# Optimization experiments

Hardware: AMD Instinct MI355X
Metric: run time of the kernel (lower is better)

Reference implementation:

```python
import jax, jax.numpy as jnp
import numpy as np

N = 262144      # total nodes
G = 256         # graphs
P = 1024        # nodes per graph (k=None sort pool keeps all)
E = 4194304     # edges
F_IN = 128
H = 32
C = 10          # out capsules / classes
OUT_LEN = 16
IN_LEN = 96     # 3 * 32 concat
NUM_ITERS = 3


def setup_inputs() -> dict:
    key = jax.random.key(0)
    ks = jax.random.split(key, 12)
    x = jax.random.normal(ks[0], (N, F_IN), jnp.float32)
    # edges within each graph of size P
    src = jax.random.randint(ks[1], (E,), 0, N)
    off = jax.random.randint(ks[2], (E,), 0, P)
    dst = (src // P) * P + off
    edge_index = jnp.stack([src, dst]).astype(jnp.int64)
    batch = jnp.repeat(jnp.arange(G), P).astype(jnp.int64)
    W1 = jax.random.normal(ks[3], (F_IN, H), jnp.float32) / np.sqrt(F_IN)
    b1 = jnp.zeros((H,), jnp.float32)
    W2 = jax.random.normal(ks[4], (H, H), jnp.float32) / np.sqrt(H)
    b2 = jnp.zeros((H,), jnp.float32)
    W3 = jax.random.normal(ks[5], (H, H), jnp.float32) / np.sqrt(H)
    b3 = jnp.zeros((H,), jnp.float32)
    caps_W = jax.random.normal(ks[6], (C, OUT_LEN, IN_LEN), jnp.float32) * 0.05
    return {"x": x, "edge_index": edge_index, "batch": batch,
            "W1": W1, "b1": b1, "W2": W2, "b2": b2, "W3": W3, "b3": b3,
            "caps_W": caps_W}


def _position_encoding(length, dim):
    pos = jnp.arange(length, dtype=jnp.float32)[:, None]
    i = jnp.arange(dim // 2, dtype=jnp.float32)[None, :]
    ang = pos / jnp.power(10000.0, 2.0 * i / dim)
    return jnp.stack([jnp.sin(ang), jnp.cos(ang)], axis=-1).reshape(length, dim)


def _squash(v, eps=1e-12):
    n2 = jnp.sum(v * v, axis=-1, keepdims=True)
    return (n2 / (1.0 + n2)) * v / jnp.sqrt(n2 + eps)


def reference(x, edge_index, batch, W1, b1, W2, b2, W3, b3, caps_W):
    src, dst = edge_index[0], edge_index[1]
    # remove_self_loops, then GCNConv re-adds self loops with weight 1
    mask = (src != dst).astype(x.dtype)
    deg = jax.ops.segment_sum(mask, dst, num_segments=N) + 1.0
    dis = jax.lax.rsqrt(deg)                         # deg^{-1/2}
    enorm = dis[src] * dis[dst] * mask               # [E]

    def gcn(h, W, b):
        h = h @ W                                    # [N,H]
        agg = jax.ops.segment_sum(h[src] * enorm[:, None], dst, num_segments=N)
        agg = agg + h * (dis * dis)[:, None]         # self-loop term deg^{-1}
        return jnp.tanh(agg + b)

    x1 = gcn(x, W1, b1)
    x2 = gcn(x1, W2, b2)
    x3 = gcn(x2, W3, b3)
    h = jnp.concatenate([x1, x2, x3], axis=-1)       # [N, 96]

    # global_sort_pool (k=None): per-graph sort by last channel, descending
    hg = h.reshape(G, P, IN_LEN)
    order = jnp.argsort(-hg[:, :, -1], axis=1)
    hs = jnp.take_along_axis(hg, order[:, :, None], axis=1)  # [G,P,96]
    hs = hs + _position_encoding(P, IN_LEN)[None]

    # CapsuleLinear, shared weight: priors [G, C, P, OUT_LEN]
    priors = jnp.einsum('oji,gki->gokj', caps_W, hs)

    # k-means routing
    v = jnp.mean(priors, axis=2, keepdims=True)      # [G,C,1,OUT_LEN]
    for _ in range(NUM_ITERS):
        vn = v / (jnp.linalg.norm(v, axis=-1, keepdims=True) + 1e-12)
        logits = jnp.sum(priors * vn, axis=-1, keepdims=True)  # [G,C,P,1]
        prob = jax.nn.softmax(logits, axis=2)
        v = jnp.sum(prob * priors, axis=2, keepdims=True)
    out = _squash(v)[:, :, 0, :]                     # [G, C, OUT_LEN]
    return jnp.linalg.norm(out, axis=-1)             # [G, C]
```

## Files before the change

### kernel.cpp

```cpp
#include <hip/hip_runtime.h>
#include <hip/hip_fp16.h>
#include <cstdint>
#include <cstddef>

#define N_NODES   262144
#define NG        256
#define PP        1024
#define NE        4194304
#define FIN       128
#define HH        32
#define NC        10
#define OL        16
#define IL        96
#define NITER     3
#define ECHUNK    4096
#define NCHUNK    (NE/ECHUNK)
#define ECAP      18432

typedef _Float16 half8 __attribute__((ext_vector_type(8)));
typedef float f32x4 __attribute__((ext_vector_type(4)));

__device__ __forceinline__ float tanh_fast(float x) {
  float e = __expf(2.0f * x);
  return 1.0f - 2.0f / (e + 1.0f);
}
__device__ __forceinline__ unsigned pk2(float a, float b) {
  __half2 h = __floats2half2_rn(a, b);
  union { __half2 h; unsigned u; } v; v.h = h; return v.u;
}
__device__ __forceinline__ __half2 u2h2(unsigned u) {
  union { unsigned u; __half2 h; } v; v.u = u; return v.h;
}

__device__ __forceinline__ int hslc(int row, int c) {
  return row * 32 + ((c ^ ((row >> 1) & 3)) << 3);
}
__device__ __forceinline__ int hslh(int row, int halfcol) {
  return hslc(row, halfcol >> 3) + (halfcol & 7);
}

__global__ void k_hist(const int* __restrict__ ei, unsigned* __restrict__ histT) {
  __shared__ unsigned lh[NG];
  int t = threadIdx.x, b = blockIdx.x;
  lh[t] = 0;
  __syncthreads();
  int base = b * ECHUNK;
  for (int q = t; q < ECHUNK; q += 256) {
    int e = base + q;
    int s = ei[e], d = ei[NE + e];
    if (s != d) atomicAdd(&lh[s >> 10], 1u);
  }
  __syncthreads();
  histT[t * NCHUNK + b] = lh[t];
}

__global__ void k_scanA(const unsigned* __restrict__ histT, unsigned* __restrict__ cbaseT,
                        unsigned* __restrict__ gtot) {
  __shared__ unsigned wtot[4];
  int t = threadIdx.x, g = blockIdx.x;
  int lane = t & 63, wv = t >> 6;
  uint4 hv = *(const uint4*)(histT + (size_t)g * NCHUNK + t * 4);
  unsigned s0 = hv.x, s1 = s0 + hv.y, s2 = s1 + hv.z, s3 = s2 + hv.w;
  unsigned tsum = s3, sc = tsum;
  for (int d = 1; d < 64; d <<= 1) {
    unsigned v = __shfl_up(sc, d, 64);
    if (lane >= d) sc += v;
  }
  if (lane == 63) wtot[wv] = sc;
  __syncthreads();
  unsigned woff = 0;
  for (int w = 0; w < wv; ++w) woff += wtot[w];
  unsigned base = woff + sc - tsum;
  cbaseT[(size_t)(t * 4 + 0) * NG + g] = base;
  cbaseT[(size_t)(t * 4 + 1) * NG + g] = base + s0;
  cbaseT[(size_t)(t * 4 + 2) * NG + g] = base + s1;
  cbaseT[(size_t)(t * 4 + 3) * NG + g] = base + s2;
  if (t == 255) gtot[g] = woff + sc;
}

__global__ void k_scanB(const unsigned* __restrict__ gtot, unsigned* __restrict__ gbase) {
  __shared__ unsigned wtot[4];
  int t = threadIdx.x;
  int lane = t & 63, wv = t >> 6;
  unsigned x = gtot[t], sc = x;
  for (int d = 1; d < 64; d <<= 1) {
    unsigned v = __shfl_up(sc, d, 64);
    if (lane >= d) sc += v;
  }
  if (lane == 63) wtot[wv] = sc;
  __syncthreads();
  unsigned woff = 0;
  for (int w = 0; w < wv; ++w) woff += wtot[w];
  gbase[t] = woff + sc - x;
  if (t == 255) gbase[256] = woff + sc;
}

__global__ void k_scatter(const int* __restrict__ ei, const unsigned* __restrict__ cbaseT,
                          const unsigned* __restrict__ gbase, unsigned* __restrict__ epack) {
  __shared__ unsigned lcur[NG];
  int t = threadIdx.x, b = blockIdx.x;
  lcur[t] = gbase[t] + cbaseT[(size_t)b * NG + t];
  __syncthreads();
  int base = b * ECHUNK;
  for (int q = t; q < ECHUNK; q += 256) {
    int e = base + q;
    int s = ei[e], d = ei[NE + e];
    if (s != d) {
      int g = s >> 10;
      unsigned pos = atomicAdd(&lcur[g], 1u);
      epack[pos] = (unsigned)(s & 1023) | ((unsigned)(d & 1023) << 10);
    }
  }
}

__global__ __launch_bounds__(256) void k_dstsort(const unsigned* __restrict__ epack,
                          const unsigned* __restrict__ gbase,
                          unsigned short* __restrict__ esrc16,
                          unsigned* __restrict__ dstptr) {
  __shared__ unsigned shist[PP];
  __shared__ unsigned wsum[256];
  __shared__ unsigned cur[PP];
  int t = threadIdx.x, g = blockIdx.x;
  unsigned e0 = gbase[g], e1 = gbase[g + 1];
  for (int i = t; i < PP; i += 256) shist[i] = 0;
  __syncthreads();
  for (unsigned e = e0 + t; e < e1; e += 256)
    atomicAdd(&shist[(epack[e] >> 10) & 1023], 1u);
  __syncthreads();
  unsigned h0 = shist[4 * t], h1 = shist[4 * t + 1], h2 = shist[4 * t + 2], h3 = shist[4 * t + 3];
  unsigned tsum = h0 + h1 + h2 + h3;
  wsum[t] = tsum;
  __syncthreads();
  for (int off = 1; off < 256; off <<= 1) {
    unsigned v = (t >= off) ? wsum[t - off] : 0u;
    __syncthreads();
    wsum[t] += v;
    __syncthreads();
  }
  unsigned excl = wsum[t] - tsum;
  unsigned c0 = excl, c1 = c0 + h0, c2 = c1 + h1, c3 = c2 + h2;
  cur[4 * t] = c0; cur[4 * t + 1] = c1; cur[4 * t + 2] = c2; cur[4 * t + 3] = c3;
  unsigned* dp = dstptr + (size_t)g * (PP + 1);
  dp[4 * t] = c0; dp[4 * t + 1] = c1; dp[4 * t + 2] = c2; dp[4 * t + 3] = c3;
  if (t == 0) dp[PP] = e1 - e0;
  __syncthreads();
  unsigned short* eg = esrc16 + (size_t)g * ECAP;
  for (unsigned e = e0 + t; e < e1; e += 256) {
    unsigned pk = epack[e];
    unsigned so = pk & 1023, dofs = (pk >> 10) & 1023;
    unsigned pos = atomicAdd(&cur[dofs], 1u);
    if (pos < ECAP) eg[pos] = (unsigned short)so;
  }
}

__global__ void k_dis(const unsigned* __restrict__ dstptr, float* __restrict__ dis) {
  int n = blockIdx.x * 256 + threadIdx.x;
  int g = n >> 10, k = n & 1023;
  const unsigned* dp = dstptr + (size_t)g * (PP + 1) + k;
  float deg = (float)(dp[1] - dp[0]);
  dis[n] = 1.0f / sqrtf(deg + 1.0f);
}

__device__ __forceinline__ void gcn_layer(__half* hsl, const float* dg, const unsigned* dp,
                                          const unsigned short* eg, const float* bias,
                                          int coloff, const float* Wn, __half* hb16,
                                          float* keyArr, int t) {
  unsigned xnu[2][16];
#pragma unroll
  for (int pth = 0; pth < 2; ++pth) {
    int k = t + pth * 512;
    float dk = dg[k];
    unsigned e0 = dp[k], e1 = dp[k + 1];
    if (e1 > (unsigned)ECAP) e1 = ECAP;
    __half2 acc2[16];
    {
      uint4 u0 = *(const uint4*)&hsl[hslc(k, 0)];
      uint4 u1 = *(const uint4*)&hsl[hslc(k, 1)];
      uint4 u2 = *(const uint4*)&hsl[hslc(k, 2)];
      uint4 u3 = *(const uint4*)&hsl[hslc(k, 3)];
      acc2[0] = u2h2(u0.x); acc2[1] = u2h2(u0.y); acc2[2] = u2h2(u0.z); acc2[3] = u2h2(u0.w);
      acc2[4] = u2h2(u1.x); acc2[5] = u2h2(u1.y); acc2[6] = u2h2(u1.z); acc2[7] = u2h2(u1.w);
      acc2[8] = u2h2(u2.x); acc2[9] = u2h2(u2.y); acc2[10] = u2h2(u2.z); acc2[11] = u2h2(u2.w);
      acc2[12] = u2h2(u3.x); acc2[13] = u2h2(u3.y); acc2[14] = u2h2(u3.z); acc2[15] = u2h2(u3.w);
    }
    unsigned e = e0;
    for (; e + 1 < e1; e += 2) {
      int s0 = eg[e], s1 = eg[e + 1];
      uint4 a0 = *(const uint4*)&hsl[hslc(s0, 0)];
      uint4 a1 = *(const uint4*)&hsl[hslc(s0, 1)];
      uint4 a2 = *(const uint4*)&hsl[hslc(s0, 2)];
      uint4 a3 = *(const uint4*)&hsl[hslc(s0, 3)];
      uint4 b0 = *(const uint4*)&hsl[hslc(s1, 0)];
      uint4 b1 = *(const uint4*)&hsl[hslc(s1, 1)];
      uint4 b2 = *(const uint4*)&hsl[hslc(s1, 2)];
      uint4 b3 = *(const uint4*)&hsl[hslc(s1, 3)];
      acc2[0] = __hadd2(acc2[0], __hadd2(u2h2(a0.x), u2h2(b0.x)));
      acc2[1] = __hadd2(acc2[1], __hadd2(u2h2(a0.y), u2h2(b0.y)));
      acc2[2] = __hadd2(acc2[2], __hadd2(u2h2(a0.z), u2h2(b0.z)));
      acc2[3] = __hadd2(acc2[3], __hadd2(u2h2(a0.w), u2h2(b0.w)));
      acc2[4] = __hadd2(acc2[4], __hadd2(u2h2(a1.x), u2h2(b1.x)));
      acc2[5] = __hadd2(acc2[5], __hadd2(u2h2(a1.y), u2h2(b1.y)));
      acc2[6] = __hadd2(acc2[6], __hadd2(u2h2(a1.z), u2h2(b1.z)));
      acc2[7] = __hadd2(acc2[7], __hadd2(u2h2(a1.w), u2h2(b1.w)));
      acc2[8] = __hadd2(acc2[8], __hadd2(u2h2(a2.x), u2h2(b2.x)));
      acc2[9] = __hadd2(acc2[9], __hadd2(u2h2(a2.y), u2h2(b2.y)));
      acc2[10] = __hadd2(acc2[10], __hadd2(u2h2(a2.z), u2h2(b2.z)));
      acc2[11] = __hadd2(acc2[11], __hadd2(u2h2(a2.w), u2h2(b2.w)));
      acc2[12] = __hadd2(acc2[12], __hadd2(u2h2(a3.x), u2h2(b3.x)));
      acc2[13] = __hadd2(acc2[13], __hadd2(u2h2(a3.y), u2h2(b3.y)));
      acc2[14] = __hadd2(acc2[14], __hadd2(u2h2(a3.z), u2h2(b3.z)));
      acc2[15] = __hadd2(acc2[15], __hadd2(u2h2(a3.w), u2h2(b3.w)));
    }
    if (e < e1) {
      int s0 = eg[e];
      uint4 a0 = *(const uint4*)&hsl[hslc(s0, 0)];
      uint4 a1 = *(const uint4*)&hsl[hslc(s0, 1)];
      uint4 a2 = *(const uint4*)&hsl[hslc(s0, 2)];
      uint4 a3 = *(const uint4*)&hsl[hslc(s0, 3)];
      acc2[0] = __hadd2(acc2[0], u2h2(a0.x)); acc2[1] = __hadd2(acc2[1], u2h2(a0.y));
      acc2[2] = __hadd2(acc2[2], u2h2(a0.z)); acc2[3] = __hadd2(acc2[3], u2h2(a0.w));
      acc2[4] = __hadd2(acc2[4], u2h2(a1.x)); acc2[5] = __hadd2(acc2[5], u2h2(a1.y));
      acc2[6] = __hadd2(acc2[6], u2h2(a1.z)); acc2[7] = __hadd2(acc2[7], u2h2(a1.w));
      acc2[8] = __hadd2(acc2[8], u2h2(a2.x)); acc2[9] = __hadd2(acc2[9], u2h2(a2.y));
      acc2[10] = __hadd2(acc2[10], u2h2(a2.z)); acc2[11] = __hadd2(acc2[11], u2h2(a2.w));
      acc2[12] = __hadd2(acc2[12], u2h2(a3.x)); acc2[13] = __hadd2(acc2[13], u2h2(a3.y));
      acc2[14] = __hadd2(acc2[14], u2h2(a3.z)); acc2[15] = __hadd2(acc2[15], u2h2(a3.w));
    }
    float lastv = 0.f;
#pragma unroll
    for (int i = 0; i < 16; ++i) {
      float2 f = __half22float2(acc2[i]);
      float a0 = tanh_fast(dk * f.x + bias[2 * i]);
      float a1 = tanh_fast(dk * f.y + bias[2 * i + 1]);
      xnu[pth][i] = pk2(a0, a1);
      if (i == 15) lastv = a1;
    }
    __half* hr = hb16 + (size_t)k * IL + coloff;
    uint4 h0, h1;
    h0.x = xnu[pth][0]; h0.y = xnu[pth][1]; h0.z = xnu[pth][2]; h0.w = xnu[pth][3];
    h1.x = xnu[pth][4]; h1.y = xnu[pth][5]; h1.z = xnu[pth][6]; h1.w = xnu[pth][7];
    ((uint4*)hr)[0] = h0;
    ((uint4*)hr)[1] = h1;
    uint4 h2, h3;
    h2.x = xnu[pth][8]; h2.y = xnu[pth][9]; h2.z = xnu[pth][10]; h2.w = xnu[pth][11];
    h3.x = xnu[pth][12]; h3.y = xnu[pth][13]; h3.z = xnu[pth][14]; h3.w = xnu[pth][15];
    ((uint4*)hr)[2] = h2;
    ((uint4*)hr)[3] = h3;
    if (keyArr) keyArr[k] = lastv;
  }
  __syncthreads();
  if (Wn) {
#pragma unroll
    for (int pth = 0; pth < 2; ++pth) {
      int k = t + pth * 512;
      float dk = dg[k];
      float4 o4[8];
#pragma unroll
      for (int j = 0; j < 8; ++j) { o4[j].x = 0.f; o4[j].y = 0.f; o4[j].z = 0.f; o4[j].w = 0.f; }
#pragma unroll
      for (int c2 = 0; c2 < 16; ++c2) {
        float2 xc = __half22float2(u2h2(xnu[pth][c2]));
        const float4* wr0 = (const float4*)(Wn + (2 * c2) * 32);
        const float4* wr1 = (const float4*)(Wn + (2 * c2 + 1) * 32);
#pragma unroll
        for (int j4 = 0; j4 < 8; ++j4) {
          float4 w0 = wr0[j4], w1 = wr1[j4];
          o4[j4].x += xc.x * w0.x + xc.y * w1.x;
          o4[j4].y += xc.x * w0.y + xc.y * w1.y;
          o4[j4].z += xc.x * w0.z + xc.y * w1.z;
          o4[j4].w += xc.x * w0.w + xc.y * w1.w;
        }
      }
#pragma unroll
      for (int c = 0; c < 4; ++c) {
        uint4 u;
        u.x = pk2(o4[2 * c].x * dk, o4[2 * c].y * dk);
        u.y = pk2(o4[2 * c].z * dk, o4[2 * c].w * dk);
        u.z = pk2(o4[2 * c + 1].x * dk, o4[2 * c + 1].y * dk);
        u.w = pk2(o4[2 * c + 1].z * dk, o4[2 * c + 1].w * dk);
        *(uint4*)&hsl[hslc(k, c)] = u;
      }
    }
    __syncthreads();
  }
}

__global__ __launch_bounds__(512, 4) void k_gcn(const float* __restrict__ x,
                                             const float* __restrict__ dis,
                                             const unsigned short* __restrict__ esrc16,
                                             const unsigned* __restrict__ dstptr,
                                             const float* __restrict__ W1, const float* __restrict__ b1,
                                             const float* __restrict__ W2, const float* __restrict__ b2,
                                             const float* __restrict__ W3, const float* __restrict__ b3,
                                             __half* __restrict__ h16, float* __restrict__ key) {
  __shared__ __half hsl[PP * 32];
  int t = threadIdx.x, g = blockIdx.x;
  const float* dg = dis + (size_t)g * PP;
  const unsigned* dp = dstptr + (size_t)g * (PP + 1);
  const unsigned short* eg = esrc16 + (size_t)g * ECAP;
  __half* hb16 = h16 + (size_t)g * PP * IL;
  float* keyg = key + (size_t)g * PP;

  {
    int wv = t >> 6, lane = t & 63, quad = lane >> 4, l16 = lane & 15;
    half8 bfr[2][4];
#pragma unroll
    for (int nt = 0; nt < 2; ++nt)
#pragma unroll
      for (int kf = 0; kf < 4; ++kf) {
        half8 bb;
#pragma unroll
        for (int j = 0; j < 8; ++j)
          bb[j] = (_Float16)W1[(kf * 32 + quad * 8 + j) * HH + nt * 16 + l16];
        bfr[nt][kf] = bb;
      }
#pragma unroll
    for (int rt = 0; rt < 8; ++rt) {
      int row = wv * 128 + rt * 16 + l16;
      const float* xr = x + ((size_t)g * PP + row) * FIN;
      half8 af[4];
#pragma unroll
      for (int kf = 0; kf < 4; ++kf) {
        float4 xa = *(const float4*)(xr + kf * 32 + quad * 8);
        float4 xb = *(const float4*)(xr + kf * 32 + quad * 8 + 4);
        half8 a;
        a[0] = (_Float16)xa.x; a[1] = (_Float16)xa.y; a[2] = (_Float16)xa.z; a[3] = (_Float16)xa.w;
        a[4] = (_Float16)xb.x; a[5] = (_Float16)xb.y; a[6] = (_Float16)xb.z; a[7] = (_Float16)xb.w;
        af[kf] = a;
      }
      int rb = wv * 128 + rt * 16 + quad * 4;
      float dv0 = dg[rb], dv1 = dg[rb + 1], dv2 = dg[rb + 2], dv3 = dg[rb + 3];
#pragma unroll
      for (int nt = 0; nt < 2; ++nt) {
        f32x4 acc = {0.f, 0.f, 0.f, 0.f};
        acc = __builtin_amdgcn_mfma_f32_16x16x32_f16(af[0], bfr[nt][0], acc, 0, 0, 0);
        acc = __builtin_amdgcn_mfma_f32_16x16x32_f16(af[1], bfr[nt][1], acc, 0, 0, 0);
        acc = __builtin_amdgcn_mfma_f32_16x16x32_f16(af[2], bfr[nt][2], acc, 0, 0, 0);
        acc = __builtin_amdgcn_mfma_f32_16x16x32_f16(af[3], bfr[nt][3], acc, 0, 0, 0);
        int col = nt * 16 + l16;
        hsl[hslh(rb + 0, col)] = __float2half(acc[0] * dv0);
        hsl[hslh(rb + 1, col)] = __float2half(acc[1] * dv1);
        hsl[hslh(rb + 2, col)] = __float2half(acc[2] * dv2);
        hsl[hslh(rb + 3, col)] = __float2half(acc[3] * dv3);
      }
    }
  }
  __syncthreads();

  gcn_layer(hsl, dg, dp, eg, b1, 0,  W2, hb16, nullptr, t);
  gcn_layer(hsl, dg, dp, eg, b2, 32, W3, hb16, nullptr, t);
  gcn_layer(hsl, dg, dp, eg, b3, 64, nullptr, hb16, keyg, t);
}

__global__ __launch_bounds__(512) void k_sort(const float* __restrict__ keyArr,
                                              unsigned short* __restrict__ rank16) {
  __shared__ float key[PP];
  __shared__ unsigned sidx[PP];
  int t = threadIdx.x, g = blockIdx.x;
  for (int i = t; i < PP; i += 512) {
    key[i] = keyArr[(size_t)g * PP + i];
    sidx[i] = i;
  }
  __syncthreads();
  for (int sz = 2; sz <= PP; sz <<= 1) {
    for (int st = sz >> 1; st > 0; st >>= 1) {
      int i = 2 * t - (t & (st - 1));
      int j = i + st;
      float ki = key[i], kj = key[j];
      unsigned ii = sidx[i], ij = sidx[j];
      bool less_ji = (kj > ki) || (kj == ki && ij < ii);
      bool asc = ((i & sz) == 0);
      if (less_ji == asc) { key[i] = kj; key[j] = ki; sidx[i] = ij; sidx[j] = ii; }
      __syncthreads();
    }
  }
  for (int i = t; i < PP; i += 512) rank16[g * PP + sidx[i]] = (unsigned short)i;
}

__global__ void k_pe(float* __restrict__ pe) {
  int id = blockIdx.x * 256 + threadIdx.x;
  if (id >= PP * 48) return;
  int pos = id / 48, i = id % 48;
  float denom = powf(10000.0f, (2.0f * i) / 96.0f);
  float ang = (float)pos / denom;
  pe[pos * IL + 2 * i] = sinf(ang);
  pe[pos * IL + 2 * i + 1] = cosf(ang);
}

__global__ void k_wpe(const float* __restrict__ pe, const float* __restrict__ capsW,
                      __half* __restrict__ wpe) {
  int id = blockIdx.x * 256 + threadIdx.x;
  if (id >= NC * PP * OL) return;
  int j = id & 15;
  int pos = (id >> 4) & 1023;
  int c = id >> 14;
  const float* wr = capsW + (size_t)(c * OL + j) * IL;
  const float* pr = pe + (size_t)pos * IL;
  float a = 0;
#pragma unroll 8
  for (int i = 0; i < IL; ++i) a += wr[i] * pr[i];
  wpe[(((size_t)c << 10) + pos) * 16 + j] = __float2half(a);
}

__global__ __launch_bounds__(256) void k_pgemm(const __half* __restrict__ h16,
                                               const float* __restrict__ capsW,
                                               __half* __restrict__ Pc) {
  int t = threadIdx.x, b = blockIdx.x;
  int g = b >> 2;
  int wv = t >> 6, lane = t & 63;
  int quad = lane >> 4, l16 = lane & 15;
  half8 afr[4][3];
#pragma unroll
  for (int rt = 0; rt < 4; ++rt) {
    int row = b * 256 + wv * 64 + rt * 16 + l16;
    const __half* hr = h16 + (size_t)row * IL + quad * 8;
#pragma unroll
    for (int kb = 0; kb < 3; ++kb) {
      uint4 u = *(const uint4*)(hr + kb * 32);
      afr[rt][kb] = __builtin_bit_cast(half8, u);
    }
  }
  int krow_base = (b & 3) * 256 + wv * 64;
  for (int ct = 0; ct < NC; ++ct) {
    half8 bfr[3];
    const float* wr = capsW + (size_t)(ct * 16 + l16) * IL + quad * 8;
#pragma unroll
    for (int kb = 0; kb < 3; ++kb) {
      float4 xx = *(const float4*)(wr + kb * 32);
      float4 yy = *(const float4*)(wr + kb * 32 + 4);
      half8 bb;
      bb[0] = (_Float16)xx.x; bb[1] = (_Float16)xx.y; bb[2] = (_Float16)xx.z; bb[3] = (_Float16)xx.w;
      bb[4] = (_Float16)yy.x; bb[5] = (_Float16)yy.y; bb[6] = (_Float16)yy.z; bb[7] = (_Float16)yy.w;
      bfr[kb] = bb;
    }
#pragma unroll
    for (int rt = 0; rt < 4; ++rt) {
      f32x4 acc = {0.f, 0.f, 0.f, 0.f};
      acc = __builtin_amdgcn_mfma_f32_16x16x32_f16(afr[rt][0], bfr[0], acc, 0, 0, 0);
      acc = __builtin_amdgcn_mfma_f32_16x16x32_f16(afr[rt][1], bfr[1], acc, 0, 0, 0);
      acc = __builtin_amdgcn_mfma_f32_16x16x32_f16(afr[rt][2], bfr[2], acc, 0, 0, 0);
      int krow = krow_base + rt * 16;
      __half* po = Pc + ((((size_t)g * NC + ct) << 10) + krow) * 16 + l16;
#pragma unroll
      for (int r = 0; r < 4; ++r)
        po[(quad * 4 + r) * 16] = __float2half(acc[r]);
    }
  }
}

__global__ __launch_bounds__(256) void k_route2(const __half* __restrict__ Pc,
                                                const __half* __restrict__ wpe,
                                                const unsigned short* __restrict__ rank16,
                                                float* __restrict__ out) {
  __shared__ float v_l[16];
  __shared__ float wred[4][17];
  int t = threadIdx.x;
  int gc = blockIdx.x;
  int g = gc / NC, c = gc - g * NC;
  int lane = t & 63, wv = t >> 6;
  const __half* pg = Pc + ((size_t)gc << 10) * 16;
  const unsigned short* rk = rank16 + (size_t)g * PP;
  const __half* wc = wpe + ((size_t)c << 10) * 16;
  float pr[4][16];
  float vsum[16];
#pragma unroll
  for (int i = 0; i < 16; ++i) vsum[i] = 0.f;
#pragma unroll
  for (int r = 0; r < 4; ++r) {
    int k = t + r * 256;
    uint4 a0 = *(const uint4*)(pg + (size_t)k * 16);
    uint4 a1 = *(const uint4*)(pg + (size_t)k * 16 + 8);
    int rkk = rk[k];
    uint4 b0 = *(const uint4*)(wc + (size_t)rkk * 16);
    uint4 b1 = *(const uint4*)(wc + (size_t)rkk * 16 + 8);
    const __half2* pa0 = (const __half2*)&a0; const __half2* pa1 = (const __half2*)&a1;
    const __half2* pb0 = (const __half2*)&b0; const __half2* pb1 = (const __half2*)&b1;
#pragma unroll
    for (int j = 0; j < 4; ++j) {
      float2 fa = __half22float2(pa0[j]); float2 fb = __half22float2(pb0[j]);
      pr[r][2 * j] = fa.x + fb.x; pr[r][2 * j + 1] = fa.y + fb.y;
      float2 fa1 = __half22float2(pa1[j]); float2 fb1 = __half22float2(pb1[j]);
      pr[r][8 + 2 * j] = fa1.x + fb1.x; pr[r][8 + 2 * j + 1] = fa1.y + fb1.y;
    }
#pragma unroll
    for (int i = 0; i < 16; ++i) vsum[i] += pr[r][i];
  }
#pragma unroll
  for (int d = 1; d < 64; d <<= 1)
#pragma unroll
    for (int i = 0; i < 16; ++i) vsum[i] += __shfl_xor(vsum[i], d, 64);
  if (lane == 0) {
#pragma unroll
    for (int i = 0; i < 16; ++i) wred[wv][i] = vsum[i];
  }
  __syncthreads();
  if (t < 16) v_l[t] = wred[0][t] + wred[1][t] + wred[2][t] + wred[3][t];
  __syncthreads();
  for (int it = 0; it < NITER; ++it) {
    float vn[16]; float n2 = 0;
#pragma unroll
    for (int i = 0; i < 16; ++i) { float x = v_l[i]; vn[i] = x; n2 += x * x; }
    float inv = 1.0f / (sqrtf(n2) + 1e-12f);
#pragma unroll
    for (int i = 0; i < 16; ++i) vn[i] *= inv;
    float lg[4];
#pragma unroll
    for (int r = 0; r < 4; ++r) {
      float a = 0;
#pragma unroll
      for (int i = 0; i < 16; ++i) a += pr[r][i] * vn[i];
      lg[r] = a;
    }
    float mx = fmaxf(fmaxf(lg[0], lg[1]), fmaxf(lg[2], lg[3]));
#pragma unroll
    for (int d = 1; d < 64; d <<= 1) mx = fmaxf(mx, __shfl_xor(mx, d, 64));
    __syncthreads();
    if (lane == 0) wred[wv][16] = mx;
    __syncthreads();
    float gmax = fmaxf(fmaxf(wred[0][16], wred[1][16]), fmaxf(wred[2][16], wred[3][16]));
    float es = 0; float eacc[16];
#pragma unroll
    for (int i = 0; i < 16; ++i) eacc[i] = 0.f;
#pragma unroll
    for (int r = 0; r < 4; ++r) {
      float e = __expf(lg[r] - gmax);
      es += e;
#pragma unroll
      for (int i = 0; i < 16; ++i) eacc[i] += e * pr[r][i];
    }
#pragma unroll
    for (int d = 1; d < 64; d <<= 1) {
      es += __shfl_xor(es, d, 64);
#pragma unroll
      for (int i = 0; i < 16; ++i) eacc[i] += __shfl_xor(eacc[i], d, 64);
    }
    __syncthreads();
    if (lane == 0) {
#pragma unroll
      for (int i = 0; i < 16; ++i) wred[wv][i] = eacc[i];
      wred[wv][16] = es;
    }
    __syncthreads();
    if (t < 16) {
      float s = wred[0][t] + wred[1][t] + wred[2][t] + wred[3][t];
      float S = wred[0][16] + wred[1][16] + wred[2][16] + wred[3][16];
      v_l[t] = s / S;
    }
    __syncthreads();
  }
  if (t == 0) {
    float n2 = 0;
#pragma unroll
    for (int i = 0; i < 16; ++i) { float x = v_l[i]; n2 += x * x; }
    out[gc] = (n2 / (1.0f + n2)) * sqrtf(n2) / sqrtf(n2 + 1e-12f);
  }
}

extern "C" void kernel_launch(void* const* d_in, const int* in_sizes, int n_in,
                              void* d_out, int out_size, void* d_ws, size_t ws_size,
                              hipStream_t stream) {
  const float* x     = (const float*)d_in[0];
  const int*   ei    = (const int*)d_in[1];
  const float* W1    = (const float*)d_in[3];
  const float* b1    = (const float*)d_in[4];
  const float* W2    = (const float*)d_in[5];
  const float* b2    = (const float*)d_in[6];
  const float* W3    = (const float*)d_in[7];
  const float* b3    = (const float*)d_in[8];
  const float* capsW = (const float*)d_in[9];
  float* out = (float*)d_out;

  char* wp = (char*)d_ws;
  auto alloc = [&](size_t bytes) { char* p = wp; wp += (bytes + 255) & ~(size_t)255; return p; };
  float*    dis    = (float*)alloc((size_t)N_NODES * 4);
  __half*   h16    = (__half*)alloc((size_t)N_NODES * IL * 2);
  float*    key    = (float*)alloc((size_t)N_NODES * 4);
  char*     ureg   = wp;
  unsigned* epack  = (unsigned*)alloc((size_t)NE * 4);
  unsigned short* esrc16 = (unsigned short*)alloc((size_t)NG * ECAP * 2);
  unsigned* histT  = (unsigned*)alloc((size_t)NCHUNK * NG * 4);
  unsigned* cbaseT = (unsigned*)alloc((size_t)NCHUNK * NG * 4);
  const size_t PC_BYTES = (size_t)NG * NC * PP * 16 * 2;
  if ((size_t)(wp - ureg) < PC_BYTES) wp = ureg + ((PC_BYTES + 255) & ~(size_t)255);
  __half*   Pc     = (__half*)ureg;
  unsigned* gtot   = (unsigned*)alloc((size_t)NG * 4);
  unsigned* gbase  = (unsigned*)alloc((size_t)(NG + 1) * 4);
  unsigned* dstptr = (unsigned*)alloc((size_t)NG * (PP + 1) * 4);
  unsigned short* rank16 = (unsigned short*)alloc((size_t)NG * PP * 2);
  float*    pe     = (float*)alloc((size_t)PP * IL * 4);
  __half*   wpe    = (__half*)alloc((size_t)NC * PP * OL * 2);

  k_hist<<<NCHUNK, 256, 0, stream>>>(ei, histT);
  k_scanA<<<NG, 256, 0, stream>>>(histT, cbaseT, gtot);
  k_scanB<<<1, 256, 0, stream>>>(gtot, gbase);
  k_scatter<<<NCHUNK, 256, 0, stream>>>(ei, cbaseT, gbase, epack);
  k_dstsort<<<NG, 256, 0, stream>>>(epack, gbase, esrc16, dstptr);
  k_dis<<<N_NODES / 256, 256, 0, stream>>>(dstptr, dis);
  k_pe<<<(PP * 48) / 256, 256, 0, stream>>>(pe);
  k_wpe<<<(NC * PP * OL) / 256, 256, 0, stream>>>(pe, capsW, wpe);

  k_gcn<<<NG, 512, 0, stream>>>(x, dis, esrc16, dstptr, W1, b1, W2, b2, W3, b3, h16, key);

  k_sort<<<NG, 512, 0, stream>>>(key, rank16);
  k_pgemm<<<N_NODES / 256, 256, 0, stream>>>(h16, capsW, Pc);
  k_route2<<<NG * NC, 256, 0, stream>>>(Pc, wpe, rank16, out);
}
```

Before: 654.2 us.

## Split fused per-graph GCN kernel into GEMM plus per-layer aggregation kernels

Replaces the single k_gcn kernel (one 512-thread block per graph running all three layers) with a standalone MFMA GEMM kernel for layer 1 and three aggregation launches. Each aggregation launch uses two blocks per graph, so 512 blocks instead of 256, which fills more compute units. The cost is an extra global round trip: each block reloads the graph's 1024x32 fp16 features into LDS, both half-blocks load the full graph, and the next layer's linear output goes through global memory in ping-pong buffers, one of which aliases the epack scratch. It also adds three extra kernel launches.

```diff
diff --git a/kernel.cpp b/kernel.cpp
--- a/kernel.cpp
+++ b/kernel.cpp
@@ -35,9 +35,6 @@
 __device__ __forceinline__ int hslc(int row, int c) {
   return row * 32 + ((c ^ ((row >> 1) & 3)) << 3);
 }
-__device__ __forceinline__ int hslh(int row, int halfcol) {
-  return hslc(row, halfcol >> 3) + (halfcol & 7);
-}
 
 __global__ void k_hist(const int* __restrict__ ei, unsigned* __restrict__ histT) {
   __shared__ unsigned lh[NG];
@@ -161,195 +158,189 @@
   dis[n] = 1.0f / sqrtf(deg + 1.0f);
 }
 
-__device__ __forceinline__ void gcn_layer(__half* hsl, const float* dg, const unsigned* dp,
-                                          const unsigned short* eg, const float* bias,
-                                          int coloff, const float* Wn, __half* hb16,
-                                          float* keyArr, int t) {
-  unsigned xnu[2][16];
-#pragma unroll
-  for (int pth = 0; pth < 2; ++pth) {
-    int k = t + pth * 512;
-    float dk = dg[k];
-    unsigned e0 = dp[k], e1 = dp[k + 1];
-    if (e1 > (unsigned)ECAP) e1 = ECAP;
-    __half2 acc2[16];
-    {
-      uint4 u0 = *(const uint4*)&hsl[hslc(k, 0)];
-      uint4 u1 = *(const uint4*)&hsl[hslc(k, 1)];
-      uint4 u2 = *(const uint4*)&hsl[hslc(k, 2)];
-      uint4 u3 = *(const uint4*)&hsl[hslc(k, 3)];
-      acc2[0] = u2h2(u0.x); acc2[1] = u2h2(u0.y); acc2[2] = u2h2(u0.z); acc2[3] = u2h2(u0.w);
-      acc2[4] = u2h2(u1.x); acc2[5] = u2h2(u1.y); acc2[6] = u2h2(u1.z); acc2[7] = u2h2(u1.w);
-      acc2[8] = u2h2(u2.x); acc2[9] = u2h2(u2.y); acc2[10] = u2h2(u2.z); acc2[11] = u2h2(u2.w);
-      acc2[12] = u2h2(u3.x); acc2[13] = u2h2(u3.y); acc2[14] = u2h2(u3.z); acc2[15] = u2h2(u3.w);
-    }
-    unsigned e = e0;
-    for (; e + 1 < e1; e += 2) {
-      int s0 = eg[e], s1 = eg[e + 1];
-      uint4 a0 = *(const uint4*)&hsl[hslc(s0, 0)];
-      uint4 a1 = *(const uint4*)&hsl[hslc(s0, 1)];
-      uint4 a2 = *(const uint4*)&hsl[hslc(s0, 2)];
-      uint4 a3 = *(const uint4*)&hsl[hslc(s0, 3)];
-      uint4 b0 = *(const uint4*)&hsl[hslc(s1, 0)];
-      uint4 b1 = *(const uint4*)&hsl[hslc(s1, 1)];
-      uint4 b2 = *(const uint4*)&hsl[hslc(s1, 2)];
-      uint4 b3 = *(const uint4*)&hsl[hslc(s1, 3)];
-      acc2[0] = __hadd2(acc2[0], __hadd2(u2h2(a0.x), u2h2(b0.x)));
-      acc2[1] = __hadd2(acc2[1], __hadd2(u2h2(a0.y), u2h2(b0.y)));
-      acc2[2] = __hadd2(acc2[2], __hadd2(u2h2(a0.z), u2h2(b0.z)));
-      acc2[3] = __hadd2(acc2[3], __hadd2(u2h2(a0.w), u2h2(b0.w)));
-      acc2[4] = __hadd2(acc2[4], __hadd2(u2h2(a1.x), u2h2(b1.x)));
-      acc2[5] = __hadd2(acc2[5], __hadd2(u2h2(a1.y), u2h2(b1.y)));
-      acc2[6] = __hadd2(acc2[6], __hadd2(u2h2(a1.z), u2h2(b1.z)));
-      acc2[7] = __hadd2(acc2[7], __hadd2(u2h2(a1.w), u2h2(b1.w)));
-      acc2[8] = __hadd2(acc2[8], __hadd2(u2h2(a2.x), u2h2(b2.x)));
-      acc2[9] = __hadd2(acc2[9], __hadd2(u2h2(a2.y), u2h2(b2.y)));
-      acc2[10] = __hadd2(acc2[10], __hadd2(u2h2(a2.z), u2h2(b2.z)));
-      acc2[11] = __hadd2(acc2[11], __hadd2(u2h2(a2.w), u2h2(b2.w)));
-      acc2[12] = __hadd2(acc2[12], __hadd2(u2h2(a3.x), u2h2(b3.x)));
-      acc2[13] = __hadd2(acc2[13], __hadd2(u2h2(a3.y), u2h2(b3.y)));
-      acc2[14] = __hadd2(acc2[14], __hadd2(u2h2(a3.z), u2h2(b3.z)));
-      acc2[15] = __hadd2(acc2[15], __hadd2(u2h2(a3.w), u2h2(b3.w)));
-    }
-    if (e < e1) {
-      int s0 = eg[e];
-      uint4 a0 = *(const uint4*)&hsl[hslc(s0, 0)];
-      uint4 a1 = *(const uint4*)&hsl[hslc(s0, 1)];
-      uint4 a2 = *(const uint4*)&hsl[hslc(s0, 2)];
-      uint4 a3 = *(const uint4*)&hsl[hslc(s0, 3)];
-      acc2[0] = __hadd2(acc2[0], u2h2(a0.x)); acc2[1] = __hadd2(acc2[1], u2h2(a0.y));
-      acc2[2] = __hadd2(acc2[2], u2h2(a0.z)); acc2[3] = __hadd2(acc2[3], u2h2(a0.w));
-      acc2[4] = __hadd2(acc2[4], u2h2(a1.x)); acc2[5] = __hadd2(acc2[5], u2h2(a1.y));
-      acc2[6] = __hadd2(acc2[6], u2h2(a1.z)); acc2[7] = __hadd2(acc2[7], u2h2(a1.w));
-      acc2[8] = __hadd2(acc2[8], u2h2(a2.x)); acc2[9] = __hadd2(acc2[9], u2h2(a2.y));
-      acc2[10] = __hadd2(acc2[10], u2h2(a2.z)); acc2[11] = __hadd2(acc2[11], u2h2(a2.w));
-      acc2[12] = __hadd2(acc2[12], u2h2(a3.x)); acc2[13] = __hadd2(acc2[13], u2h2(a3.y));
-      acc2[14] = __hadd2(acc2[14], u2h2(a3.z)); acc2[15] = __hadd2(acc2[15], u2h2(a3.w));
-    }
-    float lastv = 0.f;
-#pragma unroll
-    for (int i = 0; i < 16; ++i) {
-      float2 f = __half22float2(acc2[i]);
-      float a0 = tanh_fast(dk * f.x + bias[2 * i]);
-      float a1 = tanh_fast(dk * f.y + bias[2 * i + 1]);
-      xnu[pth][i] = pk2(a0, a1);
-      if (i == 15) lastv = a1;
-    }
-    __half* hr = hb16 + (size_t)k * IL + coloff;
-    uint4 h0, h1;
-    h0.x = xnu[pth][0]; h0.y = xnu[pth][1]; h0.z = xnu[pth][2]; h0.w = xnu[pth][3];
-    h1.x = xnu[pth][4]; h1.y = xnu[pth][5]; h1.z = xnu[pth][6]; h1.w = xnu[pth][7];
-    ((uint4*)hr)[0] = h0;
-    ((uint4*)hr)[1] = h1;
-    uint4 h2, h3;
-    h2.x = xnu[pth][8]; h2.y = xnu[pth][9]; h2.z = xnu[pth][10]; h2.w = xnu[pth][11];
-    h3.x = xnu[pth][12]; h3.y = xnu[pth][13]; h3.z = xnu[pth][14]; h3.w = xnu[pth][15];
-    ((uint4*)hr)[2] = h2;
-    ((uint4*)hr)[3] = h3;
-    if (keyArr) keyArr[k] = lastv;
-  }
-  __syncthreads();
-  if (Wn) {
-#pragma unroll
-    for (int pth = 0; pth < 2; ++pth) {
-      int k = t + pth * 512;
-      float dk = dg[k];
-      float4 o4[8];
-#pragma unroll
-      for (int j = 0; j < 8; ++j) { o4[j].x = 0.f; o4[j].y = 0.f; o4[j].z = 0.f; o4[j].w = 0.f; }
-#pragma unroll
-      for (int c2 = 0; c2 < 16; ++c2) {
-        float2 xc = __half22float2(u2h2(xnu[pth][c2]));
-        const float4* wr0 = (const float4*)(Wn + (2 * c2) * 32);
-        const float4* wr1 = (const float4*)(Wn + (2 * c2 + 1) * 32);
-#pragma unroll
-        for (int j4 = 0; j4 < 8; ++j4) {
-          float4 w0 = wr0[j4], w1 = wr1[j4];
-          o4[j4].x += xc.x * w0.x + xc.y * w1.x;
-          o4[j4].y += xc.x * w0.y + xc.y * w1.y;
-          o4[j4].z += xc.x * w0.z + xc.y * w1.z;
-          o4[j4].w += xc.x * w0.w + xc.y * w1.w;
-        }
-      }
-#pragma unroll
-      for (int c = 0; c < 4; ++c) {
-        uint4 u;
-        u.x = pk2(o4[2 * c].x * dk, o4[2 * c].y * dk);
-        u.y = pk2(o4[2 * c].z * dk, o4[2 * c].w * dk);
-        u.z = pk2(o4[2 * c + 1].x * dk, o4[2 * c + 1].y * dk);
-        u.w = pk2(o4[2 * c + 1].z * dk, o4[2 * c + 1].w * dk);
-        *(uint4*)&hsl[hslc(k, c)] = u;
-      }
-    }
-    __syncthreads();
-  }
-}
-
-__global__ __launch_bounds__(512, 4) void k_gcn(const float* __restrict__ x,
-                                             const float* __restrict__ dis,
-                                             const unsigned short* __restrict__ esrc16,
-                                             const unsigned* __restrict__ dstptr,
-                                             const float* __restrict__ W1, const float* __restrict__ b1,
-                                             const float* __restrict__ W2, const float* __restrict__ b2,
-                                             const float* __restrict__ W3, const float* __restrict__ b3,
-                                             __half* __restrict__ h16, float* __restrict__ key) {
+__global__ __launch_bounds__(256) void k_gemm1(const float* __restrict__ x,
+                                               const float* __restrict__ dis,
+                                               const float* __restrict__ W1,
+                                               __half* __restrict__ hlin) {
+  int t = threadIdx.x, b = blockIdx.x;
+  int wv = t >> 6, lane = t & 63, quad = lane >> 4, l16 = lane & 15;
+  half8 bfr[2][4];
+#pragma unroll
+  for (int nt = 0; nt < 2; ++nt)
+#pragma unroll
+    for (int kf = 0; kf < 4; ++kf) {
+      half8 bb;
+#pragma unroll
+      for (int j = 0; j < 8; ++j)
+        bb[j] = (_Float16)W1[(kf * 32 + quad * 8 + j) * HH + nt * 16 + l16];
+      bfr[nt][kf] = bb;
+    }
+#pragma unroll
+  for (int rt = 0; rt < 4; ++rt) {
+    int row = b * 256 + wv * 64 + rt * 16 + l16;
+    const float* xr = x + (size_t)row * FIN;
+    half8 af[4];
+#pragma unroll
+    for (int kf = 0; kf < 4; ++kf) {
+      float4 xa = *(const float4*)(xr + kf * 32 + quad * 8);
+      float4 xb = *(const float4*)(xr + kf * 32 + quad * 8 + 4);
+      half8 a;
+      a[0] = (_Float16)xa.x; a[1] = (_Float16)xa.y; a[2] = (_Float16)xa.z; a[3] = (_Float16)xa.w;
+      a[4] = (_Float16)xb.x; a[5] = (_Float16)xb.y; a[6] = (_Float16)xb.z; a[7] = (_Float16)xb.w;
+      af[kf] = a;
+    }
+    int rb = b * 256 + wv * 64 + rt * 16 + quad * 4;
+    float dv0 = dis[rb], dv1 = dis[rb + 1], dv2 = dis[rb + 2], dv3 = dis[rb + 3];
+#pragma unroll
+    for (int nt = 0; nt < 2; ++nt) {
+      f32x4 acc = {0.f, 0.f, 0.f, 0.f};
+      acc = __builtin_amdgcn_mfma_f32_16x16x32_f16(af[0], bfr[nt][0], acc, 0, 0, 0);
+      acc = __builtin_amdgcn_mfma_f32_16x16x32_f16(af[1], bfr[nt][1], acc, 0, 0, 0);
+      acc = __builtin_amdgcn_mfma_f32_16x16x32_f16(af[2], bfr[nt][2], acc, 0, 0, 0);
+      acc = __builtin_amdgcn_mfma_f32_16x16x32_f16(af[3], bfr[nt][3], acc, 0, 0, 0);
+      int col = nt * 16 + l16;
+      hlin[(size_t)(rb + 0) * HH + col] = __float2half(acc[0] * dv0);
+      hlin[(size_t)(rb + 1) * HH + col] = __float2half(acc[1] * dv1);
+      hlin[(size_t)(rb + 2) * HH + col] = __float2half(acc[2] * dv2);
+      hlin[(size_t)(rb + 3) * HH + col] = __float2half(acc[3] * dv3);
+    }
+  }
+}
+
+__global__ __launch_bounds__(512, 1) void k_agg(const __half* __restrict__ hlin,
+                                                const float* __restrict__ dis,
+                                                const unsigned short* __restrict__ esrc16,
+                                                const unsigned* __restrict__ dstptr,
+                                                const float* __restrict__ bias,
+                                                int coloff,
+                                                const float* __restrict__ Wn,
+                                                __half* __restrict__ h16,
+                                                __half* __restrict__ hlin_next,
+                                                float* __restrict__ keyArr) {
   __shared__ __half hsl[PP * 32];
-  int t = threadIdx.x, g = blockIdx.x;
-  const float* dg = dis + (size_t)g * PP;
+  int t = threadIdx.x;
+  int g = blockIdx.x >> 1, half = blockIdx.x & 1;
+  const uint4* src = (const uint4*)(hlin + (size_t)g * PP * HH);
+#pragma unroll
+  for (int i = 0; i < 8; ++i) {
+    int p = t + i * 512;
+    uint4 v = src[p];
+    *(uint4*)&hsl[hslc(p >> 2, p & 3)] = v;
+  }
+  __syncthreads();
+
+  int k = half * 512 + t;
+  float dk = dis[(size_t)g * PP + k];
   const unsigned* dp = dstptr + (size_t)g * (PP + 1);
   const unsigned short* eg = esrc16 + (size_t)g * ECAP;
-  __half* hb16 = h16 + (size_t)g * PP * IL;
-  float* keyg = key + (size_t)g * PP;
-
+  unsigned e0 = dp[k], e1 = dp[k + 1];
+  if (e1 > (unsigned)ECAP) e1 = ECAP;
+  __half2 acc2[16];
   {
-    int wv = t >> 6, lane = t & 63, quad = lane >> 4, l16 = lane & 15;
-    half8 bfr[2][4];
-#pragma unroll
-    for (int nt = 0; nt < 2; ++nt)
-#pragma unroll
-      for (int kf = 0; kf < 4; ++kf) {
-        half8 bb;
-#pragma unroll
-        for (int j = 0; j < 8; ++j)
-          bb[j] = (_Float16)W1[(kf * 32 + quad * 8 + j) * HH + nt * 16 + l16];
-        bfr[nt][kf] = bb;
+    uint4 u0 = *(const uint4*)&hsl[hslc(k, 0)];
+    uint4 u1 = *(const uint4*)&hsl[hslc(k, 1)];
+    uint4 u2 = *(const uint4*)&hsl[hslc(k, 2)];
+    uint4 u3 = *(const uint4*)&hsl[hslc(k, 3)];
+    acc2[0] = u2h2(u0.x); acc2[1] = u2h2(u0.y); acc2[2] = u2h2(u0.z); acc2[3] = u2h2(u0.w);
+    acc2[4] = u2h2(u1.x); acc2[5] = u2h2(u1.y); acc2[6] = u2h2(u1.z); acc2[7] = u2h2(u1.w);
+    acc2[8] = u2h2(u2.x); acc2[9] = u2h2(u2.y); acc2[10] = u2h2(u2.z); acc2[11] = u2h2(u2.w);
+    acc2[12] = u2h2(u3.x); acc2[13] = u2h2(u3.y); acc2[14] = u2h2(u3.z); acc2[15] = u2h2(u3.w);
+  }
+  unsigned e = e0;
+  for (; e + 1 < e1; e += 2) {
+    int s0 = eg[e], s1 = eg[e + 1];
+    uint4 a0 = *(const uint4*)&hsl[hslc(s0, 0)];
+    uint4 a1 = *(const uint4*)&hsl[hslc(s0, 1)];
+    uint4 a2 = *(const uint4*)&hsl[hslc(s0, 2)];
+    uint4 a3 = *(const uint4*)&hsl[hslc(s0, 3)];
+    uint4 b0 = *(const uint4*)&hsl[hslc(s1, 0)];
+    uint4 b1 = *(const uint4*)&hsl[hslc(s1, 1)];
+    uint4 b2 = *(const uint4*)&hsl[hslc(s1, 2)];
+    uint4 b3 = *(const uint4*)&hsl[hslc(s1, 3)];
+    acc2[0] = __hadd2(acc2[0], __hadd2(u2h2(a0.x), u2h2(b0.x)));
+    acc2[1] = __hadd2(acc2[1], __hadd2(u2h2(a0.y), u2h2(b0.y)));
+    acc2[2] = __hadd2(acc2[2], __hadd2(u2h2(a0.z), u2h2(b0.z)));
+    acc2[3] = __hadd2(acc2[3], __hadd2(u2h2(a0.w), u2h2(b0.w)));
+    acc2[4] = __hadd2(acc2[4], __hadd2(u2h2(a1.x), u2h2(b1.x)));
+    acc2[5] = __hadd2(acc2[5], __hadd2(u2h2(a1.y), u2h2(b1.y)));
+    acc2[6] = __hadd2(acc2[6], __hadd2(u2h2(a1.z), u2h2(b1.z)));
+    acc2[7] = __hadd2(acc2[7], __hadd2(u2h2(a1.w), u2h2(b1.w)));
+    acc2[8] = __hadd2(acc2[8], __hadd2(u2h2(a2.x), u2h2(b2.x)));
+    acc2[9] = __hadd2(acc2[9], __hadd2(u2h2(a2.y), u2h2(b2.y)));
+    acc2[10] = __hadd2(acc2[10], __hadd2(u2h2(a2.z), u2h2(b2.z)));
+    acc2[11] = __hadd2(acc2[11], __hadd2(u2h2(a2.w), u2h2(b2.w)));
+    acc2[12] = __hadd2(acc2[12], __hadd2(u2h2(a3.x), u2h2(b3.x)));
+    acc2[13] = __hadd2(acc2[13], __hadd2(u2h2(a3.y), u2h2(b3.y)));
+    acc2[14] = __hadd2(acc2[14], __hadd2(u2h2(a3.z), u2h2(b3.z)));
+    acc2[15] = __hadd2(acc2[15], __hadd2(u2h2(a3.w), u2h2(b3.w)));
+  }
+  if (e < e1) {
+    int s0 = eg[e];
+    uint4 a0 = *(const uint4*)&hsl[hslc(s0, 0)];
+    uint4 a1 = *(const uint4*)&hsl[hslc(s0, 1)];
+    uint4 a2 = *(const uint4*)&hsl[hslc(s0, 2)];
+    uint4 a3 = *(const uint4*)&hsl[hslc(s0, 3)];
+    acc2[0] = __hadd2(acc2[0], u2h2(a0.x)); acc2[1] = __hadd2(acc2[1], u2h2(a0.y));
+    acc2[2] = __hadd2(acc2[2], u2h2(a0.z)); acc2[3] = __hadd2(acc2[3], u2h2(a0.w));
+    acc2[4] = __hadd2(acc2[4], u2h2(a1.x)); acc2[5] = __hadd2(acc2[5], u2h2(a1.y));
+    acc2[6] = __hadd2(acc2[6], u2h2(a1.z)); acc2[7] = __hadd2(acc2[7], u2h2(a1.w));
+    acc2[8] = __hadd2(acc2[8], u2h2(a2.x)); acc2[9] = __hadd2(acc2[9], u2h2(a2.y));
+    acc2[10] = __hadd2(acc2[10], u2h2(a2.z)); acc2[11] = __hadd2(acc2[11], u2h2(a2.w));
+    acc2[12] = __hadd2(acc2[12], u2h2(a3.x)); acc2[13] = __hadd2(acc2[13], u2h2(a3.y));
+    acc2[14] = __hadd2(acc2[14], u2h2(a3.z)); acc2[15] = __hadd2(acc2[15], u2h2(a3.w));
+  }
+  unsigned xnu[16];
+  float lastv = 0.f;
+#pragma unroll
+  for (int i = 0; i < 16; ++i) {
+    float2 f = __half22float2(acc2[i]);
+    float a0 = tanh_fast(dk * f.x + bias[2 * i]);
+    float a1 = tanh_fast(dk * f.y + bias[2 * i + 1]);
+    xnu[i] = pk2(a0, a1);
+    if (i == 15) lastv = a1;
+  }
+  __half* hr = h16 + (size_t)((size_t)g * PP + k) * IL + coloff;
+  {
+    uint4 h0, h1, h2, h3;
+    h0.x = xnu[0]; h0.y = xnu[1]; h0.z = xnu[2]; h0.w = xnu[3];
+    h1.x = xnu[4]; h1.y = xnu[5]; h1.z = xnu[6]; h1.w = xnu[7];
+    h2.x = xnu[8]; h2.y = xnu[9]; h2.z = xnu[10]; h2.w = xnu[11];
+    h3.x = xnu[12]; h3.y = xnu[13]; h3.z = xnu[14]; h3.w = xnu[15];
+    ((uint4*)hr)[0] = h0; ((uint4*)hr)[1] = h1;
+    ((uint4*)hr)[2] = h2; ((uint4*)hr)[3] = h3;
+  }
+  if (keyArr) keyArr[(size_t)g * PP + k] = lastv;
+  if (Wn) {
+    float4 o4[8];
+#pragma unroll
+    for (int j = 0; j < 8; ++j) { o4[j].x = 0.f; o4[j].y = 0.f; o4[j].z = 0.f; o4[j].w = 0.f; }
+#pragma unroll
+    for (int c2 = 0; c2 < 16; ++c2) {
+      float2 xc = __half22float2(u2h2(xnu[c2]));
+      const float4* wr0 = (const float4*)(Wn + (2 * c2) * 32);
+      const float4* wr1 = (const float4*)(Wn + (2 * c2 + 1) * 32);
+#pragma unroll
+      for (int j4 = 0; j4 < 8; ++j4) {
+        float4 w0 = wr0[j4], w1 = wr1[j4];
+        o4[j4].x += xc.x * w0.x + xc.y * w1.x;
+        o4[j4].y += xc.x * w0.y + xc.y * w1.y;
+        o4[j4].z += xc.x * w0.z + xc.y * w1.z;
+        o4[j4].w += xc.x * w0.w + xc.y * w1.w;
       }
-#pragma unroll
-    for (int rt = 0; rt < 8; ++rt) {
-      int row = wv * 128 + rt * 16 + l16;
-      const float* xr = x + ((size_t)g * PP + row) * FIN;
-      half8 af[4];
-#pragma unroll
-      for (int kf = 0; kf < 4; ++kf) {
-        float4 xa = *(const float4*)(xr + kf * 32 + quad * 8);
-        float4 xb = *(const float4*)(xr + kf * 32 + quad * 8 + 4);
-        half8 a;
-        a[0] = (_Float16)xa.x; a[1] = (_Float16)xa.y; a[2] = (_Float16)xa.z; a[3] = (_Float16)xa.w;
-        a[4] = (_Float16)xb.x; a[5] = (_Float16)xb.y; a[6] = (_Float16)xb.z; a[7] = (_Float16)xb.w;
-        af[kf] = a;
-      }
-      int rb = wv * 128 + rt * 16 + quad * 4;
-      float dv0 = dg[rb], dv1 = dg[rb + 1], dv2 = dg[rb + 2], dv3 = dg[rb + 3];
-#pragma unroll
-      for (int nt = 0; nt < 2; ++nt) {
-        f32x4 acc = {0.f, 0.f, 0.f, 0.f};
-        acc = __builtin_amdgcn_mfma_f32_16x16x32_f16(af[0], bfr[nt][0], acc, 0, 0, 0);
-        acc = __builtin_amdgcn_mfma_f32_16x16x32_f16(af[1], bfr[nt][1], acc, 0, 0, 0);
-        acc = __builtin_amdgcn_mfma_f32_16x16x32_f16(af[2], bfr[nt][2], acc, 0, 0, 0);
-        acc = __builtin_amdgcn_mfma_f32_16x16x32_f16(af[3], bfr[nt][3], acc, 0, 0, 0);
-        int col = nt * 16 + l16;
-        hsl[hslh(rb + 0, col)] = __float2half(acc[0] * dv0);
-        hsl[hslh(rb + 1, col)] = __float2half(acc[1] * dv1);
-        hsl[hslh(rb + 2, col)] = __float2half(acc[2] * dv2);
-        hsl[hslh(rb + 3, col)] = __float2half(acc[3] * dv3);
-      }
-    }
-  }
-  __syncthreads();
-
-  gcn_layer(hsl, dg, dp, eg, b1, 0,  W2, hb16, nullptr, t);
-  gcn_layer(hsl, dg, dp, eg, b2, 32, W3, hb16, nullptr, t);
-  gcn_layer(hsl, dg, dp, eg, b3, 64, nullptr, hb16, keyg, t);
+    }
+    __half* op = hlin_next + (size_t)((size_t)g * PP + k) * HH;
+    uint4 u0, u1, u2, u3;
+    u0.x = pk2(o4[0].x * dk, o4[0].y * dk); u0.y = pk2(o4[0].z * dk, o4[0].w * dk);
+    u0.z = pk2(o4[1].x * dk, o4[1].y * dk); u0.w = pk2(o4[1].z * dk, o4[1].w * dk);
+    u1.x = pk2(o4[2].x * dk, o4[2].y * dk); u1.y = pk2(o4[2].z * dk, o4[2].w * dk);
+    u1.z = pk2(o4[3].x * dk, o4[3].y * dk); u1.w = pk2(o4[3].z * dk, o4[3].w * dk);
+    u2.x = pk2(o4[4].x * dk, o4[4].y * dk); u2.y = pk2(o4[4].z * dk, o4[4].w * dk);
+    u2.z = pk2(o4[5].x * dk, o4[5].y * dk); u2.w = pk2(o4[5].z * dk, o4[5].w * dk);
+    u3.x = pk2(o4[6].x * dk, o4[6].y * dk); u3.y = pk2(o4[6].z * dk, o4[6].w * dk);
+    u3.z = pk2(o4[7].x * dk, o4[7].y * dk); u3.w = pk2(o4[7].z * dk, o4[7].w * dk);
+    ((uint4*)op)[0] = u0; ((uint4*)op)[1] = u1;
+    ((uint4*)op)[2] = u2; ((uint4*)op)[3] = u3;
+  }
 }
 
 __global__ __launch_bounds__(512) void k_sort(const float* __restrict__ keyArr,
@@ -577,6 +568,8 @@
   float*    key    = (float*)alloc((size_t)N_NODES * 4);
   char*     ureg   = wp;
   unsigned* epack  = (unsigned*)alloc((size_t)NE * 4);
+  __half*   hlinA  = (__half*)epack;
+  __half*   hlinB  = (__half*)alloc((size_t)N_NODES * HH * 2);
   unsigned short* esrc16 = (unsigned short*)alloc((size_t)NG * ECAP * 2);
   unsigned* histT  = (unsigned*)alloc((size_t)NCHUNK * NG * 4);
   unsigned* cbaseT = (unsigned*)alloc((size_t)NCHUNK * NG * 4);
@@ -599,7 +592,10 @@
   k_pe<<<(PP * 48) / 256, 256, 0, stream>>>(pe);
   k_wpe<<<(NC * PP * OL) / 256, 256, 0, stream>>>(pe, capsW, wpe);
 
-  k_gcn<<<NG, 512, 0, stream>>>(x, dis, esrc16, dstptr, W1, b1, W2, b2, W3, b3, h16, key);
+  k_gemm1<<<N_NODES / 256, 256, 0, stream>>>(x, dis, W1, hlinA);
+  k_agg<<<NG * 2, 512, 0, stream>>>(hlinA, dis, esrc16, dstptr, b1, 0,  W2, h16, hlinB, nullptr);
+  k_agg<<<NG * 2, 512, 0, stream>>>(hlinB, dis, esrc16, dstptr, b2, 32, W3, h16, hlinA, nullptr);
+  k_agg<<<NG * 2, 512, 0, stream>>>(hlinA, dis, esrc16, dstptr, b3, 64, nullptr, h16, nullptr, key);
 
   k_sort<<<NG, 512, 0, stream>>>(key, rank16);
   k_pgemm<<<N_NODES / 256, 256, 0, stream>>>(h16, capsW, Pc);
```

After: 564.7 us. -13.7%, faster.
